# Kernel tuning notes

Hardware: AMD Instinct MI355X
Metric: run time of the kernel (lower is better)

Reference implementation:

```python
import jax, jax.numpy as jnp
import numpy as np

EPS = 1e-5  # matches module default eps


def setup_inputs() -> dict:
    key = jax.random.key(0)
    n, F = 4096, 256
    k1, k2, k3, k4, k5 = jax.random.split(key, 5)
    # Orthonormal eigenbasis (eigh of a symmetric Laplacian yields orthogonal V)
    V = jnp.linalg.qr(jax.random.normal(k1, (n, n), dtype=jnp.float32))[0]
    # Nonnegative Laplacian spectrum with lam[0] = 0 (module asserts sqrtlam[0] ~ 0)
    lam = jnp.sort(jax.random.uniform(k2, (n,), dtype=jnp.float32) * 4.0)
    lam = lam.at[0].set(0.0)
    x = jax.random.normal(k3, (n, F, 1), dtype=jnp.float32)
    y = jax.random.normal(k4, (n, F, 1), dtype=jnp.float32)
    t = jnp.float32(0.7)
    return {"x": x, "y": y, "t": t, "lam": lam, "V": V}


def reference(x, y, t, lam, V):
    # safe_sqrt: clamp tiny negatives (|lam|<eps) to zero before sqrt
    sqrtlam = jnp.sqrt(jnp.maximum(lam, 0.0))
    # P1 spectrum: cos(t * sqrt(lam))
    c = jnp.cos(t * sqrtlam)
    # P2 spectrum: sin(t*s)/s with limit t as s->0 (safe_P2_eigh)
    small = jnp.abs(sqrtlam) < EPS
    safe_s = jnp.where(small, 1.0, sqrtlam)
    p2 = jnp.where(small, t, jnp.sin(t * safe_s) / safe_s)

    def apply_spectral(d, sig):
        # (V diag(d) V^T) @ sig, contracted over node axis; sig: [n, F, C]
        vt_sig = jnp.einsum('ji,jfc->ifc', V, sig)          # V^T @ sig
        return jnp.einsum('ij,jfc->ifc', V, d[:, None, None] * vt_sig)

    # res1 + res2: P1 @ x + P2 @ y (the scatter-add message passing with all
    # nonzeros of the dense P matrices is exactly this dense mat-vec)
    return apply_spectral(c, x) + apply_spectral(p2, y)
```

## Files before the change

kernel.cpp:

```cpp
#include <hip/hip_runtime.h>

typedef __attribute__((ext_vector_type(8))) short short8;
typedef __attribute__((ext_vector_type(8))) unsigned short ushort8v;
typedef __attribute__((ext_vector_type(4))) float f32x4;

#define N_NODES 4096
#define N_FEAT  256

__device__ __forceinline__ unsigned short f2bf(float f) {
  union { float f; unsigned u; } a; a.f = f;
  unsigned r = a.u + 0x7FFFu + ((a.u >> 16) & 1u);
  return (unsigned short)(r >> 16);
}

__device__ __forceinline__ float bf2f(unsigned short u) {
  union { unsigned u; float f; } a; a.u = ((unsigned)u) << 16;
  return a.f;
}

__device__ __forceinline__ void gload_lds16(const void* g, void* l) {
  __builtin_amdgcn_global_load_lds(
      (const __attribute__((address_space(1))) void*)g,
      (__attribute__((address_space(3))) void*)l, 16, 0, 0);
}

__global__ __launch_bounds__(256) void prep_all_k(const float* __restrict__ V,
                                                  const float* __restrict__ x,
                                                  const float* __restrict__ y,
                                                  unsigned short* __restrict__ Vbf,
                                                  unsigned short* __restrict__ Vt,
                                                  unsigned short* __restrict__ S2T) {
  __shared__ unsigned short smem[2][64][72];
  const int t = threadIdx.x;
  const int r = t >> 2, q = t & 3;
  const unsigned b = blockIdx.x;
  if (b < 4096u) {
    const int bx = b & 63, by = b >> 6;
    const int gr = by * 64 + r;
    const int gc0 = bx * 64;
#pragma unroll
    for (int i = 0; i < 4; ++i) {
      int c = q * 4 + i * 16;
      float4 v = *(const float4*)&V[(size_t)gr * N_NODES + gc0 + c];
      ushort4 u; u.x = f2bf(v.x); u.y = f2bf(v.y); u.z = f2bf(v.z); u.w = f2bf(v.w);
      *(ushort4*)&Vbf[(size_t)gr * N_NODES + gc0 + c] = u;
      smem[0][c + 0][r] = u.x; smem[0][c + 1][r] = u.y;
      smem[0][c + 2][r] = u.z; smem[0][c + 3][r] = u.w;
    }
    __syncthreads();
    const int r2 = t >> 2;
#pragma unroll
    for (int j = 0; j < 2; ++j) {
      int ms = q * 8 + j * 32;
      ushort8v u = *(const ushort8v*)&smem[0][r2][ms];
      *(ushort8v*)&Vt[(size_t)(gc0 + r2) * N_NODES + by * 64 + ms] = u;
    }
  } else {
    const unsigned b2 = b - 4096u;
    const int bx = b2 & 3, by = b2 >> 2;
    const int gj = by * 64 + r;
    const int gf0 = bx * 64;
#pragma unroll
    for (int i = 0; i < 4; ++i) {
      int c = q * 4 + i * 16;
      float4 vx = *(const float4*)&x[(size_t)gj * N_FEAT + gf0 + c];
      float4 vy = *(const float4*)&y[(size_t)gj * N_FEAT + gf0 + c];
      smem[0][c + 0][r] = f2bf(vx.x); smem[0][c + 1][r] = f2bf(vx.y);
      smem[0][c + 2][r] = f2bf(vx.z); smem[0][c + 3][r] = f2bf(vx.w);
      smem[1][c + 0][r] = f2bf(vy.x); smem[1][c + 1][r] = f2bf(vy.y);
      smem[1][c + 2][r] = f2bf(vy.z); smem[1][c + 3][r] = f2bf(vy.w);
    }
    __syncthreads();
    const int f2 = t >> 2;
#pragma unroll
    for (int j = 0; j < 2; ++j) {
      int js = q * 8 + j * 32;
      ushort8v ux = *(const ushort8v*)&smem[0][f2][js];
      ushort8v uy = *(const ushort8v*)&smem[1][f2][js];
      *(ushort8v*)&S2T[(size_t)(2 * (gf0 + f2) + 0) * N_NODES + by * 64 + js] = ux;
      *(ushort8v*)&S2T[(size_t)(2 * (gf0 + f2) + 1) * N_NODES + by * 64 + js] = uy;
    }
  }
}

template <int NTB>
__global__ __launch_bounds__(256, 4) void gemm_swz(const unsigned short* __restrict__ A,
                                                   const unsigned short* __restrict__ B,
                                                   unsigned short* __restrict__ part,
                                                   int K, int Kc, int Nn, size_t MN) {
  __shared__ unsigned short As[128 * 64];
  __shared__ unsigned short Bs[128 * 64];
  const int t = threadIdx.x;
  const int lane = t & 63, w = t >> 6;

  const unsigned L = blockIdx.x;
  const unsigned cx = L & 7u, j = L >> 3u;
  const unsigned ntile = j & ((1u << NTB) - 1u);
  const unsigned GPX = (gridDim.x >> 3) >> NTB;
  const unsigned group = cx * GPX + (j >> NTB);
  const unsigned mtile = group & 31u;
  const unsigned zz = group >> 5u;

  const int wr = (w >> 1) * 64;
  const int wc = (w & 1) * 64;
  const int l15 = lane & 15;
  const int lhi = lane >> 4;

  const size_t kbase = (size_t)zz * Kc;
  const size_t srcoff = (size_t)(lane >> 3) * K * 2 + (size_t)(((lane & 7) ^ (lane >> 3)) << 4);

  const char* Ag = (const char*)(A + (size_t)mtile * 128 * K + kbase);
  const char* Bg = (const char*)(B + (size_t)ntile * 128 * K + kbase);

  f32x4 acc[4][4];
#pragma unroll
  for (int mi = 0; mi < 4; ++mi)
#pragma unroll
    for (int ni = 0; ni < 4; ++ni) acc[mi][ni] = (f32x4){0.f, 0.f, 0.f, 0.f};

  const int nkt = Kc >> 6;
  for (int kt = 0; kt < nkt; ++kt) {
    const size_t ko = (size_t)kt * 128;
#pragma unroll
    for (int q = 0; q < 4; ++q)
      gload_lds16(Ag + (size_t)(w * 4 + q) * 8 * K * 2 + srcoff + ko, &As[(w * 4 + q) * 512]);
#pragma unroll
    for (int q = 0; q < 4; ++q)
      gload_lds16(Bg + (size_t)(w * 4 + q) * 8 * K * 2 + srcoff + ko, &Bs[(w * 4 + q) * 512]);
    __syncthreads();
#pragma unroll
    for (int ks = 0; ks < 2; ++ks) {
      short8 a[4], b[4];
#pragma unroll
      for (int mi = 0; mi < 4; ++mi) {
        const int ar = wr + mi * 16 + l15;
        a[mi] = *(const short8*)((const char*)As + (size_t)ar * 128 +
                                 ((((ks << 2) | lhi) ^ (ar & 7)) << 4));
      }
#pragma unroll
      for (int ni = 0; ni < 4; ++ni) {
        const int br = wc + ni * 16 + l15;
        b[ni] = *(const short8*)((const char*)Bs + (size_t)br * 128 +
                                 ((((ks << 2) | lhi) ^ (br & 7)) << 4));
      }
#pragma unroll
      for (int mi = 0; mi < 4; ++mi)
#pragma unroll
        for (int ni = 0; ni < 4; ++ni)
          acc[mi][ni] = __builtin_amdgcn_mfma_f32_16x16x32_bf16(a[mi], b[ni],
                                                                acc[mi][ni], 0, 0, 0);
    }
    __syncthreads();
  }

  unsigned short* po = part + (size_t)zz * MN;
  const int m0 = mtile * 128 + wr + lhi * 4;
  const int n0 = ntile * 128 + wc + l15;
#pragma unroll
  for (int mi = 0; mi < 4; ++mi)
#pragma unroll
    for (int ni = 0; ni < 4; ++ni)
#pragma unroll
      for (int r = 0; r < 4; ++r)
        po[(size_t)(m0 + mi * 16 + r) * Nn + n0 + ni * 16] = f2bf(acc[mi][ni][r]);
}

__global__ __launch_bounds__(256) void reduce1_k(const unsigned short* __restrict__ part,
                                                 const float* __restrict__ lam,
                                                 const float* __restrict__ tp,
                                                 unsigned short* __restrict__ Zt) {
  __shared__ unsigned short zt[64][72];
  const int t = threadIdx.x;
  const int r = t >> 2, q = t & 3;
  const int m = blockIdx.y * 64 + r;
  const int n0 = blockIdx.x * 128;
  const float tv = tp[0];
  const float s = sqrtf(fmaxf(lam[m], 0.f));
  const float cv = cosf(tv * s);
  const float pv = (s < 1e-5f) ? tv : (sinf(tv * s) / s);
  float acc[16];
#pragma unroll
  for (int i = 0; i < 16; ++i) acc[i] = 0.f;
  for (int ks = 0; ks < 8; ++ks) {
    const unsigned short* p = part + ((size_t)ks * N_NODES + m) * 512 + n0;
#pragma unroll
    for (int i = 0; i < 8; ++i) {
      ushort4 u = *(const ushort4*)&p[q * 4 + i * 16];
      acc[2 * i + 0] += cv * bf2f(u.x) + pv * bf2f(u.y);
      acc[2 * i + 1] += cv * bf2f(u.z) + pv * bf2f(u.w);
    }
  }
#pragma unroll
  for (int i = 0; i < 8; ++i) {
    int f = q * 2 + i * 8;
    zt[f + 0][r] = f2bf(acc[2 * i + 0]);
    zt[f + 1][r] = f2bf(acc[2 * i + 1]);
  }
  __syncthreads();
  const int f2 = t >> 2;
  const int gf = blockIdx.x * 64 + f2;
#pragma unroll
  for (int w = 0; w < 2; ++w) {
    int js = q * 8 + w * 32;
    ushort8v u = *(const ushort8v*)&zt[f2][js];
    *(ushort8v*)&Zt[(size_t)gf * N_NODES + blockIdx.y * 64 + js] = u;
  }
}

__global__ __launch_bounds__(256) void reduce2_k(const unsigned short* __restrict__ part,
                                                 float* __restrict__ out) {
  const size_t e = ((size_t)blockIdx.x * 256 + threadIdx.x) * 4;
  float4 s = {0.f, 0.f, 0.f, 0.f};
#pragma unroll
  for (int ks = 0; ks < 16; ++ks) {
    ushort4 u = *(const ushort4*)&part[(size_t)ks * N_NODES * N_FEAT + e];
    s.x += bf2f(u.x); s.y += bf2f(u.y); s.z += bf2f(u.z); s.w += bf2f(u.w);
  }
  *(float4*)&out[e] = s;
}

extern "C" void kernel_launch(void* const* d_in, const int* in_sizes, int n_in,
                              void* d_out, int out_size, void* d_ws, size_t ws_size,
                              hipStream_t stream) {
  const float* x   = (const float*)d_in[0];
  const float* y   = (const float*)d_in[1];
  const float* tp  = (const float*)d_in[2];
  const float* lam = (const float*)d_in[3];
  const float* V   = (const float*)d_in[4];

  char* w = (char*)d_ws;
  unsigned short* Vbf  = (unsigned short*)w; w += (size_t)N_NODES * N_NODES * 2;
  unsigned short* Vtbf = (unsigned short*)w; w += (size_t)N_NODES * N_NODES * 2;
  unsigned short* S2T  = (unsigned short*)w; w += (size_t)512 * N_NODES * 2;
  unsigned short* Zt   = (unsigned short*)w; w += (size_t)N_FEAT * N_NODES * 2;
  unsigned short* partb = (unsigned short*)w; w += (size_t)8 * N_NODES * 512 * 2;

  prep_all_k<<<4096 + 256, 256, 0, stream>>>(V, x, y, Vbf, Vtbf, S2T);
  gemm_swz<2><<<1024, 256, 0, stream>>>(Vtbf, S2T, partb, N_NODES, 512, 512,
                                        (size_t)N_NODES * 512);
  reduce1_k<<<dim3(512 / 128, N_NODES / 64), 256, 0, stream>>>(partb, lam, tp, Zt);
  gemm_swz<1><<<1024, 256, 0, stream>>>(Vbf, Zt, partb, N_NODES, 256, N_FEAT,
                                        (size_t)N_NODES * N_FEAT);
  reduce2_k<<<(N_NODES * N_FEAT) / 1024, 256, 0, stream>>>(partb, (float*)d_out);
}
```

Before: 170.8 us.

## Replace split-K partial buffers with fp32 atomic accumulation and fused spectral scaling

```diff
diff --git a/kernel.cpp b/kernel.cpp
--- a/kernel.cpp
+++ b/kernel.cpp
@@ -13,15 +13,19 @@
   return (unsigned short)(r >> 16);
 }
 
-__device__ __forceinline__ float bf2f(unsigned short u) {
-  union { unsigned u; float f; } a; a.u = ((unsigned)u) << 16;
-  return a.f;
-}
-
 __device__ __forceinline__ void gload_lds16(const void* g, void* l) {
   __builtin_amdgcn_global_load_lds(
       (const __attribute__((address_space(1))) void*)g,
       (__attribute__((address_space(3))) void*)l, 16, 0, 0);
+}
+
+__global__ void spectrum_k(const float* __restrict__ lam, const float* __restrict__ tp,
+                           float* __restrict__ cbuf, float* __restrict__ p2buf) {
+  int i = blockIdx.x * 256 + threadIdx.x;
+  float tv = tp[0];
+  float s = sqrtf(fmaxf(lam[i], 0.f));
+  cbuf[i] = cosf(tv * s);
+  p2buf[i] = (s < 1e-5f) ? tv : (sinf(tv * s) / s);
 }
 
 __global__ __launch_bounds__(256) void prep_all_k(const float* __restrict__ V,
@@ -83,11 +87,13 @@
   }
 }
 
-template <int NTB>
+template <int NTB, bool SCALE>
 __global__ __launch_bounds__(256, 4) void gemm_swz(const unsigned short* __restrict__ A,
                                                    const unsigned short* __restrict__ B,
-                                                   unsigned short* __restrict__ part,
-                                                   int K, int Kc, int Nn, size_t MN) {
+                                                   float* __restrict__ out,
+                                                   const float* __restrict__ cbuf,
+                                                   const float* __restrict__ p2buf,
+                                                   int K, int Kc, int Nn) {
   __shared__ unsigned short As[128 * 64];
   __shared__ unsigned short Bs[128 * 64];
   const int t = threadIdx.x;
@@ -153,42 +159,43 @@
     __syncthreads();
   }
 
-  unsigned short* po = part + (size_t)zz * MN;
   const int m0 = mtile * 128 + wr + lhi * 4;
   const int n0 = ntile * 128 + wc + l15;
 #pragma unroll
-  for (int mi = 0; mi < 4; ++mi)
-#pragma unroll
-    for (int ni = 0; ni < 4; ++ni)
-#pragma unroll
-      for (int r = 0; r < 4; ++r)
-        po[(size_t)(m0 + mi * 16 + r) * Nn + n0 + ni * 16] = f2bf(acc[mi][ni][r]);
-}
-
-__global__ __launch_bounds__(256) void reduce1_k(const unsigned short* __restrict__ part,
-                                                 const float* __restrict__ lam,
-                                                 const float* __restrict__ tp,
-                                                 unsigned short* __restrict__ Zt) {
+  for (int mi = 0; mi < 4; ++mi) {
+    const int m = m0 + mi * 16;
+    f32x4 cv, pv;
+    if (SCALE) {
+      cv = *(const f32x4*)&cbuf[m];
+      pv = *(const f32x4*)&p2buf[m];
+    }
+#pragma unroll
+    for (int ni = 0; ni < 4; ++ni) {
+      const int n = n0 + ni * 16;
+#pragma unroll
+      for (int r = 0; r < 4; ++r) {
+        float v = acc[mi][ni][r];
+        if (SCALE) v *= ((n & 1) ? pv[r] : cv[r]);
+        atomicAdd(&out[(size_t)(m + r) * Nn + n], v);
+      }
+    }
+  }
+}
+
+__global__ __launch_bounds__(256) void scaleT_k(const float* __restrict__ Z,
+                                                unsigned short* __restrict__ Zt) {
   __shared__ unsigned short zt[64][72];
   const int t = threadIdx.x;
   const int r = t >> 2, q = t & 3;
   const int m = blockIdx.y * 64 + r;
   const int n0 = blockIdx.x * 128;
-  const float tv = tp[0];
-  const float s = sqrtf(fmaxf(lam[m], 0.f));
-  const float cv = cosf(tv * s);
-  const float pv = (s < 1e-5f) ? tv : (sinf(tv * s) / s);
+  const float* p = Z + (size_t)m * 512 + n0;
   float acc[16];
 #pragma unroll
-  for (int i = 0; i < 16; ++i) acc[i] = 0.f;
-  for (int ks = 0; ks < 8; ++ks) {
-    const unsigned short* p = part + ((size_t)ks * N_NODES + m) * 512 + n0;
-#pragma unroll
-    for (int i = 0; i < 8; ++i) {
-      ushort4 u = *(const ushort4*)&p[q * 4 + i * 16];
-      acc[2 * i + 0] += cv * bf2f(u.x) + pv * bf2f(u.y);
-      acc[2 * i + 1] += cv * bf2f(u.z) + pv * bf2f(u.w);
-    }
+  for (int i = 0; i < 8; ++i) {
+    float4 v = *(const float4*)&p[q * 4 + i * 16];
+    acc[2 * i + 0] = v.x + v.y;
+    acc[2 * i + 1] = v.z + v.w;
   }
 #pragma unroll
   for (int i = 0; i < 8; ++i) {
@@ -205,18 +212,6 @@
     ushort8v u = *(const ushort8v*)&zt[f2][js];
     *(ushort8v*)&Zt[(size_t)gf * N_NODES + blockIdx.y * 64 + js] = u;
   }
-}
-
-__global__ __launch_bounds__(256) void reduce2_k(const unsigned short* __restrict__ part,
-                                                 float* __restrict__ out) {
-  const size_t e = ((size_t)blockIdx.x * 256 + threadIdx.x) * 4;
-  float4 s = {0.f, 0.f, 0.f, 0.f};
-#pragma unroll
-  for (int ks = 0; ks < 16; ++ks) {
-    ushort4 u = *(const ushort4*)&part[(size_t)ks * N_NODES * N_FEAT + e];
-    s.x += bf2f(u.x); s.y += bf2f(u.y); s.z += bf2f(u.z); s.w += bf2f(u.w);
-  }
-  *(float4*)&out[e] = s;
 }
 
 extern "C" void kernel_launch(void* const* d_in, const int* in_sizes, int n_in,
@@ -233,13 +228,17 @@
   unsigned short* Vtbf = (unsigned short*)w; w += (size_t)N_NODES * N_NODES * 2;
   unsigned short* S2T  = (unsigned short*)w; w += (size_t)512 * N_NODES * 2;
   unsigned short* Zt   = (unsigned short*)w; w += (size_t)N_FEAT * N_NODES * 2;
-  unsigned short* partb = (unsigned short*)w; w += (size_t)8 * N_NODES * 512 * 2;
-
+  float* Zbuf  = (float*)w; w += (size_t)N_NODES * 512 * 4;
+  float* cbuf  = (float*)w; w += N_NODES * 4;
+  float* p2buf = (float*)w; w += N_NODES * 4;
+
+  hipMemsetAsync(Zbuf, 0, (size_t)N_NODES * 512 * 4, stream);
+  hipMemsetAsync(d_out, 0, (size_t)N_NODES * N_FEAT * 4, stream);
+  spectrum_k<<<N_NODES / 256, 256, 0, stream>>>(lam, tp, cbuf, p2buf);
   prep_all_k<<<4096 + 256, 256, 0, stream>>>(V, x, y, Vbf, Vtbf, S2T);
-  gemm_swz<2><<<1024, 256, 0, stream>>>(Vtbf, S2T, partb, N_NODES, 512, 512,
-                                        (size_t)N_NODES * 512);
-  reduce1_k<<<dim3(512 / 128, N_NODES / 64), 256, 0, stream>>>(partb, lam, tp, Zt);
-  gemm_swz<1><<<1024, 256, 0, stream>>>(Vbf, Zt, partb, N_NODES, 256, N_FEAT,
-                                        (size_t)N_NODES * N_FEAT);
-  reduce2_k<<<(N_NODES * N_FEAT) / 1024, 256, 0, stream>>>(partb, (float*)d_out);
-}
+  gemm_swz<2, true><<<1024, 256, 0, stream>>>(Vtbf, S2T, Zbuf, cbuf, p2buf,
+                                              N_NODES, 512, 512);
+  scaleT_k<<<dim3(512 / 128, N_NODES / 64), 256, 0, stream>>>(Zbuf, Zt);
+  gemm_swz<1, false><<<1024, 256, 0, stream>>>(Vbf, Zt, (float*)d_out, nullptr, nullptr,
+                                               N_NODES, 256, N_FEAT);
+}
```

New measurement: 253.7 us. +48.5%, slower.

## Fuse spectral scaling and transpose into first GEMM epilogue, simplify reduction

Applied to the files above, without the earlier changes.

```diff
diff --git a/kernel.cpp b/kernel.cpp
--- a/kernel.cpp
+++ b/kernel.cpp
@@ -22,6 +22,15 @@
   __builtin_amdgcn_global_load_lds(
       (const __attribute__((address_space(1))) void*)g,
       (__attribute__((address_space(3))) void*)l, 16, 0, 0);
+}
+
+__global__ void spectrum_k(const float* __restrict__ lam, const float* __restrict__ tp,
+                           float* __restrict__ cbuf, float* __restrict__ p2buf) {
+  int i = blockIdx.x * 256 + threadIdx.x;
+  float tv = tp[0];
+  float s = sqrtf(fmaxf(lam[i], 0.f));
+  cbuf[i] = cosf(tv * s);
+  p2buf[i] = (s < 1e-5f) ? tv : (sinf(tv * s) / s);
 }
 
 __global__ __launch_bounds__(256) void prep_all_k(const float* __restrict__ V,
@@ -83,10 +92,12 @@
   }
 }
 
-template <int NTB>
+template <int NTB, bool SCALE>
 __global__ __launch_bounds__(256, 4) void gemm_swz(const unsigned short* __restrict__ A,
                                                    const unsigned short* __restrict__ B,
-                                                   unsigned short* __restrict__ part,
+                                                   unsigned short* __restrict__ outp,
+                                                   const float* __restrict__ cbuf,
+                                                   const float* __restrict__ p2buf,
                                                    int K, int Kc, int Nn, size_t MN) {
   __shared__ unsigned short As[128 * 64];
   __shared__ unsigned short Bs[128 * 64];
@@ -153,58 +164,70 @@
     __syncthreads();
   }
 
-  unsigned short* po = part + (size_t)zz * MN;
   const int m0 = mtile * 128 + wr + lhi * 4;
-  const int n0 = ntile * 128 + wc + l15;
-#pragma unroll
-  for (int mi = 0; mi < 4; ++mi)
-#pragma unroll
-    for (int ni = 0; ni < 4; ++ni)
-#pragma unroll
-      for (int r = 0; r < 4; ++r)
-        po[(size_t)(m0 + mi * 16 + r) * Nn + n0 + ni * 16] = f2bf(acc[mi][ni][r]);
-}
-
-__global__ __launch_bounds__(256) void reduce1_k(const unsigned short* __restrict__ part,
-                                                 const float* __restrict__ lam,
-                                                 const float* __restrict__ tp,
+  if (SCALE) {
+    unsigned short* tb = As;
+#pragma unroll
+    for (int mi = 0; mi < 4; ++mi) {
+      const int m = m0 + mi * 16;
+      f32x4 cv = *(const f32x4*)&cbuf[m];
+      f32x4 pv = *(const f32x4*)&p2buf[m];
+      const int mloc = wr + lhi * 4 + mi * 16;
+#pragma unroll
+      for (int ni = 0; ni < 4; ++ni) {
+        float z[4];
+#pragma unroll
+        for (int r = 0; r < 4; ++r) {
+          float own = acc[mi][ni][r];
+          float oth = __shfl_xor(own, 1);
+          z[r] = cv[r] * own + pv[r] * oth;
+        }
+        if (!(lane & 1)) {
+          const int floc = (wc >> 1) + (l15 >> 1) + ni * 8;
+          const int cm = (mloc >> 2) ^ ((floc & 7) << 2);
+          ushort4 u; u.x = f2bf(z[0]); u.y = f2bf(z[1]); u.z = f2bf(z[2]); u.w = f2bf(z[3]);
+          *(ushort4*)&tb[floc * 128 + cm * 4] = u;
+        }
+      }
+    }
+    __syncthreads();
+    unsigned short* Zs = outp + (size_t)zz * MN + (size_t)(ntile * 64) * N_NODES + mtile * 128;
+    const int fl = t >> 2, seg = t & 3;
+#pragma unroll
+    for (int jj = 0; jj < 4; ++jj) {
+      const int c = (seg * 8 + jj * 2) ^ ((fl & 7) << 2);
+      ushort8v u = *(const ushort8v*)&tb[fl * 128 + c * 4];
+      *(ushort8v*)&Zs[(size_t)fl * N_NODES + seg * 32 + jj * 8] = u;
+    }
+  } else {
+    unsigned short* po = outp + (size_t)zz * MN;
+    const int n0 = ntile * 128 + wc + l15;
+#pragma unroll
+    for (int mi = 0; mi < 4; ++mi)
+#pragma unroll
+      for (int ni = 0; ni < 4; ++ni)
+#pragma unroll
+        for (int r = 0; r < 4; ++r)
+          po[(size_t)(m0 + mi * 16 + r) * Nn + n0 + ni * 16] = f2bf(acc[mi][ni][r]);
+  }
+}
+
+__global__ __launch_bounds__(256) void reduce1_k(const unsigned short* __restrict__ Z2,
                                                  unsigned short* __restrict__ Zt) {
-  __shared__ unsigned short zt[64][72];
-  const int t = threadIdx.x;
-  const int r = t >> 2, q = t & 3;
-  const int m = blockIdx.y * 64 + r;
-  const int n0 = blockIdx.x * 128;
-  const float tv = tp[0];
-  const float s = sqrtf(fmaxf(lam[m], 0.f));
-  const float cv = cosf(tv * s);
-  const float pv = (s < 1e-5f) ? tv : (sinf(tv * s) / s);
-  float acc[16];
-#pragma unroll
-  for (int i = 0; i < 16; ++i) acc[i] = 0.f;
+  const size_t e = ((size_t)blockIdx.x * 256 + threadIdx.x) * 8;
+  float s[8];
+#pragma unroll
+  for (int i = 0; i < 8; ++i) s[i] = 0.f;
+#pragma unroll
   for (int ks = 0; ks < 8; ++ks) {
-    const unsigned short* p = part + ((size_t)ks * N_NODES + m) * 512 + n0;
-#pragma unroll
-    for (int i = 0; i < 8; ++i) {
-      ushort4 u = *(const ushort4*)&p[q * 4 + i * 16];
-      acc[2 * i + 0] += cv * bf2f(u.x) + pv * bf2f(u.y);
-      acc[2 * i + 1] += cv * bf2f(u.z) + pv * bf2f(u.w);
-    }
-  }
-#pragma unroll
-  for (int i = 0; i < 8; ++i) {
-    int f = q * 2 + i * 8;
-    zt[f + 0][r] = f2bf(acc[2 * i + 0]);
-    zt[f + 1][r] = f2bf(acc[2 * i + 1]);
-  }
-  __syncthreads();
-  const int f2 = t >> 2;
-  const int gf = blockIdx.x * 64 + f2;
-#pragma unroll
-  for (int w = 0; w < 2; ++w) {
-    int js = q * 8 + w * 32;
-    ushort8v u = *(const ushort8v*)&zt[f2][js];
-    *(ushort8v*)&Zt[(size_t)gf * N_NODES + blockIdx.y * 64 + js] = u;
-  }
+    ushort8v u = *(const ushort8v*)&Z2[(size_t)ks * N_FEAT * N_NODES + e];
+#pragma unroll
+    for (int i = 0; i < 8; ++i) s[i] += bf2f(u[i]);
+  }
+  ushort8v o;
+#pragma unroll
+  for (int i = 0; i < 8; ++i) o[i] = f2bf(s[i]);
+  *(ushort8v*)&Zt[e] = o;
 }
 
 __global__ __launch_bounds__(256) void reduce2_k(const unsigned short* __restrict__ part,
@@ -233,13 +256,18 @@
   unsigned short* Vtbf = (unsigned short*)w; w += (size_t)N_NODES * N_NODES * 2;
   unsigned short* S2T  = (unsigned short*)w; w += (size_t)512 * N_NODES * 2;
   unsigned short* Zt   = (unsigned short*)w; w += (size_t)N_FEAT * N_NODES * 2;
-  unsigned short* partb = (unsigned short*)w; w += (size_t)8 * N_NODES * 512 * 2;
-
+  float* cbuf  = (float*)w; w += N_NODES * 4;
+  float* p2buf = (float*)w; w += N_NODES * 4;
+  unsigned short* partb = (unsigned short*)w;
+
+  spectrum_k<<<N_NODES / 256, 256, 0, stream>>>(lam, tp, cbuf, p2buf);
   prep_all_k<<<4096 + 256, 256, 0, stream>>>(V, x, y, Vbf, Vtbf, S2T);
-  gemm_swz<2><<<1024, 256, 0, stream>>>(Vtbf, S2T, partb, N_NODES, 512, 512,
-                                        (size_t)N_NODES * 512);
-  reduce1_k<<<dim3(512 / 128, N_NODES / 64), 256, 0, stream>>>(partb, lam, tp, Zt);
-  gemm_swz<1><<<1024, 256, 0, stream>>>(Vbf, Zt, partb, N_NODES, 256, N_FEAT,
-                                        (size_t)N_NODES * N_FEAT);
+  gemm_swz<2, true><<<1024, 256, 0, stream>>>(Vtbf, S2T, partb, cbuf, p2buf,
+                                              N_NODES, 512, 512,
+                                              (size_t)N_FEAT * N_NODES);
+  reduce1_k<<<(N_FEAT * N_NODES) / 2048, 256, 0, stream>>>(partb, Zt);
+  gemm_swz<1, false><<<1024, 256, 0, stream>>>(Vbf, Zt, partb, nullptr, nullptr,
+                                               N_NODES, 256, N_FEAT,
+                                               (size_t)N_NODES * N_FEAT);
   reduce2_k<<<(N_NODES * N_FEAT) / 1024, 256, 0, stream>>>(partb, (float*)d_out);
 }
```

Measured after the change: 178.9 us. 4.7% more time.
